# Kernel optimization log

Hardware: AMD Instinct MI355X
Metric: run time of the kernel (lower is better)

Reference implementation:

```python
import jax, jax.numpy as jnp
import numpy as np

TEMPERATURE = 100.0  # exponential-smoothing temperature from __init__ default
ETA = 1.0            # feature/label cost tradeoff


def _cdist(a, b):
    # Euclidean distance matrix [M, N] between rows of a [M, D] and b [N, D]
    sq = (jnp.sum(a * a, axis=1)[:, None]
          + jnp.sum(b * b, axis=1)[None, :]
          - 2.0 * (a @ b.T))
    return jnp.sqrt(jnp.maximum(sq, 1e-12))


def setup_inputs() -> dict:
    key = jax.random.key(0)
    ks = jax.random.split(key, 9)
    B, Nt, Ns, H, Wd, C = 1024, 8192, 8192, 32, 32, 10
    D = H * Wd
    x = jax.random.normal(ks[0], (B, H, Wd), jnp.float32)
    target_features = jax.random.normal(ks[1], (Nt, H, Wd), jnp.float32)
    aligned_source_features = jax.random.normal(ks[2], (Nt, H, Wd), jnp.float32)
    source_features = jax.random.normal(ks[3], (Ns, H, Wd), jnp.float32)
    source_high_dim_labels = jax.random.uniform(ks[4], (Ns, C), jnp.float32)
    aligned_target_labels = jax.random.uniform(ks[5], (Ns, C), jnp.float32)
    source_label_distances = jax.random.uniform(ks[6], (C, C), jnp.float32)
    W = jax.random.normal(ks[7], (D, C), jnp.float32) * 0.02
    b = jnp.zeros((C,), jnp.float32)
    return {
        "x": x,
        "target_features": target_features,
        "aligned_source_features": aligned_source_features,
        "source_features": source_features,
        "source_high_dim_labels": source_high_dim_labels,
        "aligned_target_labels": aligned_target_labels,
        "source_label_distances": source_label_distances,
        "W": W,
        "b": b,
    }


def reference(x, target_features, aligned_source_features, source_features,
              source_high_dim_labels, aligned_target_labels,
              source_label_distances, W, b):
    B = x.shape[0]
    xf = x.reshape(B, -1)                                   # [B, D]
    tf = target_features.reshape(target_features.shape[0], -1)       # [Nt, D]
    asf = aligned_source_features.reshape(aligned_source_features.shape[0], -1)  # [Nt, D]
    sf = source_features.reshape(source_features.shape[0], -1)       # [Ns, D]

    # --- feature transport: target -> source (plain_softmax) ---
    d_feat = _cdist(xf, tf)                                 # [B, Nt]
    w_feat = jax.nn.softmax(-TEMPERATURE * d_feat, axis=1)  # [B, Nt]
    x_src = w_feat @ asf                                    # [B, D] in source space

    # --- source model (linear classifier head -> soft predictions) ---
    preds = jax.nn.softmax(x_src @ W + b, axis=1)           # [B, C]

    # --- label transport: source -> target (plain_softmax) ---
    cost = _cdist(x_src, sf)                                # feature_dists=True: [B, Ns]
    # label_dists=True: cost of moving predicted label mass to each sample's label
    cost = cost + ETA * (preds @ source_label_distances @ source_high_dim_labels.T)
    w_lab = jax.nn.softmax(-TEMPERATURE * cost, axis=1)     # [B, Ns]
    y = w_lab @ aligned_target_labels                       # [B, C] in target label space
    return y
```

## Files before the change

### kernel.cpp

```cpp
#include <hip/hip_runtime.h>
#include <hip/hip_bf16.h>
#include <math.h>

#define B_ROWS 1024
#define NT 8192
#define NS 8192
#define DIM 1024
#define NC 10
#define TEMP 100.0f
#define WCAP 1024

typedef __bf16 bf16x8 __attribute__((ext_vector_type(8)));
typedef __bf16 bf16x4 __attribute__((ext_vector_type(4)));
typedef float f32x4 __attribute__((ext_vector_type(4)));

#define GLOAD_LDS(g, l) \
    __builtin_amdgcn_global_load_lds((__attribute__((address_space(1))) void*)(g), \
                                     (__attribute__((address_space(3))) void*)(l), 16, 0, 0)

__device__ inline __bf16 split_hi(float v) { return (__bf16)v; }
__device__ inline __bf16 split_lo(float v) {
    __bf16 h = (__bf16)v;
    return (__bf16)(v - (float)h);
}

__device__ inline float wave_max(float v) {
    #pragma unroll
    for (int off = 32; off > 0; off >>= 1)
        v = fmaxf(v, __shfl_down(v, off, 64));
    return v;
}
__device__ inline float wave_sum(float v) {
    #pragma unroll
    for (int off = 32; off > 0; off >>= 1)
        v += __shfl_down(v, off, 64);
    return v;
}

__device__ inline void conv_norm_row(const float* __restrict__ X, int row,
                                     __bf16* __restrict__ X2,
                                     float* __restrict__ norms,
                                     float* sred) {
    int c = threadIdx.x * 4;
    float4 v = *(const float4*)(X + (size_t)row * DIM + c);
    bf16x4 h, l;
    h[0] = split_hi(v.x); l[0] = split_lo(v.x);
    h[1] = split_hi(v.y); l[1] = split_lo(v.y);
    h[2] = split_hi(v.z); l[2] = split_lo(v.z);
    h[3] = split_hi(v.w); l[3] = split_lo(v.w);
    *(bf16x4*)(X2 + (size_t)row * 2048 + c) = h;
    *(bf16x4*)(X2 + (size_t)row * 2048 + 1024 + c) = l;
    float acc = v.x * v.x + v.y * v.y + v.z * v.z + v.w * v.w;
    float w = wave_sum(acc);
    int lane = threadIdx.x & 63, wid = threadIdx.x >> 6;
    if (lane == 0) sred[wid] = w;
    __syncthreads();
    if (threadIdx.x == 0) norms[row] = sred[0] + sred[1] + sred[2] + sred[3];
}

__global__ __launch_bounds__(256) void k_prep0(const float* __restrict__ x,
                                               const float* __restrict__ tf,
                                               const float* __restrict__ sf,
                                               const float* __restrict__ sld,
                                               const float* __restrict__ shdl,
                                               const float* __restrict__ atl,
                                               __bf16* __restrict__ x2,
                                               __bf16* __restrict__ tf2,
                                               __bf16* __restrict__ sf2,
                                               float* __restrict__ nx_,
                                               float* __restrict__ nt_,
                                               float* __restrict__ ns_,
                                               float* __restrict__ M2Tt,
                                               float* __restrict__ atlt) {
    __shared__ float sred[4];
    __shared__ float sldL[NC * NC];
    int b = blockIdx.x;
    if (b < B_ROWS) {
        conv_norm_row(x, b, x2, nx_, sred);
    } else if (b < B_ROWS + NT) {
        conv_norm_row(tf, b - B_ROWS, tf2, nt_, sred);
    } else if (b < B_ROWS + NT + NS) {
        conv_norm_row(sf, b - B_ROWS - NT, sf2, ns_, sred);
    } else {
        if (threadIdx.x < NC * NC) sldL[threadIdx.x] = sld[threadIdx.x];
        __syncthreads();
        int j = (b - B_ROWS - NT - NS) * 256 + threadIdx.x;
        float sh[NC], at[NC];
        #pragma unroll
        for (int k = 0; k < NC; k++) sh[k] = shdl[(size_t)j * NC + k];
        #pragma unroll
        for (int c = 0; c < NC; c++) at[c] = atl[(size_t)j * NC + c];
        #pragma unroll
        for (int c = 0; c < NC; c++) {
            float t = 0.f;
            #pragma unroll
            for (int k = 0; k < NC; k++) t += sldL[c * NC + k] * sh[k];
            M2Tt[c * NS + j] = t;
            atlt[c * NS + j] = at[c];
        }
    }
}

template <bool LOGITS>
__global__ __launch_bounds__(256) void k_gemm3(const __bf16* __restrict__ A2,
                                               const __bf16* __restrict__ B2,
                                               float* __restrict__ C,
                                               int M, int N, int K, int ksplit,
                                               const float* __restrict__ rowN,
                                               const float* __restrict__ colN) {
    __shared__ unsigned short AhS[8192], AlS[8192], BhS[8192], BlS[8192];
    __shared__ float extraL[LOGITS ? 256 : 2];
    float* rnL = extraL;
    float* cnL = extraL + 128;

    int tid = threadIdx.x;
    int wid = tid >> 6, lane = tid & 63;
    int wm = (wid >> 1) * 64, wn = (wid & 1) * 64;
    int id = blockIdx.y * gridDim.x + blockIdx.x;
    int bn_i = ((id >> 6) << 3) | (id & 7);
    int bm_i = (id >> 3) & 7;
    int bm = bm_i * 128, bn = bn_i * 128;
    size_t K2 = 2 * (size_t)K;
    int k_begin = blockIdx.z * ksplit;
    int nsteps = ksplit >> 6;

    if (LOGITS) {
        if (tid < 128) rnL[tid] = rowN[bm + tid];
        else cnL[tid - 128] = colN[bn + tid - 128];
    }

    f32x4 acc[4][4];
    #pragma unroll
    for (int i = 0; i < 4; i++)
        #pragma unroll
        for (int j = 0; j < 4; j++) acc[i][j] = (f32x4){0.f, 0.f, 0.f, 0.f};

    int r_in = lane >> 3;
    int cgo = ((lane & 7) ^ r_in) * 8;
    const __bf16* gA = A2 + (size_t)(bm + wid * 32 + r_in) * K2 + k_begin + cgo;
    const __bf16* gB = B2 + (size_t)(bn + wid * 32 + r_in) * K2 + k_begin + cgo;
    char* AhB = (char*)AhS; char* AlB = (char*)AlS;
    char* BhB = (char*)BhS; char* BlB = (char*)BlS;
    int lbw = wid * 4096;
    size_t row8 = 8 * K2;

    int ra = lane & 15, q = lane >> 4;
    int aoff[4][2], boff[4][2];
    #pragma unroll
    for (int i = 0; i < 4; i++) {
        #pragma unroll
        for (int kh = 0; kh < 2; kh++) {
            int chunk = ((kh << 2) | q) ^ (ra & 7);
            aoff[i][kh] = (wm + i * 16 + ra) * 64 + chunk * 8;
            boff[i][kh] = (wn + i * 16 + ra) * 64 + chunk * 8;
        }
    }
    const __bf16* AhE = (const __bf16*)AhS;
    const __bf16* AlE = (const __bf16*)AlS;
    const __bf16* BhE = (const __bf16*)BhS;
    const __bf16* BlE = (const __bf16*)BlS;

    for (int ks = 0; ks < nsteps; ks++) {
        __syncthreads();
        #pragma unroll
        for (int p = 0; p < 4; p++) {
            size_t go = p * row8;
            int lo = lbw + p * 1024;
            GLOAD_LDS(gA + go, AhB + lo);
            GLOAD_LDS(gA + go + K, AlB + lo);
            GLOAD_LDS(gB + go, BhB + lo);
            GLOAD_LDS(gB + go + K, BlB + lo);
        }
        gA += 64; gB += 64;
        __syncthreads();

        #pragma unroll
        for (int kh = 0; kh < 2; kh++) {
            bf16x8 ah[4], al[4];
            #pragma unroll
            for (int mi = 0; mi < 4; mi++) {
                ah[mi] = *(const bf16x8*)(AhE + aoff[mi][kh]);
                al[mi] = *(const bf16x8*)(AlE + aoff[mi][kh]);
            }
            #pragma unroll
            for (int ni = 0; ni < 4; ni++) {
                bf16x8 bh = *(const bf16x8*)(BhE + boff[ni][kh]);
                bf16x8 bl = *(const bf16x8*)(BlE + boff[ni][kh]);
                #pragma unroll
                for (int mi = 0; mi < 4; mi++) {
                    acc[mi][ni] = __builtin_amdgcn_mfma_f32_16x16x32_bf16(ah[mi], bh, acc[mi][ni], 0, 0, 0);
                    acc[mi][ni] = __builtin_amdgcn_mfma_f32_16x16x32_bf16(ah[mi], bl, acc[mi][ni], 0, 0, 0);
                    acc[mi][ni] = __builtin_amdgcn_mfma_f32_16x16x32_bf16(al[mi], bh, acc[mi][ni], 0, 0, 0);
                }
            }
        }
    }

    if (!LOGITS) {
        float* Cb = C + (size_t)blockIdx.z * M * N;
        #pragma unroll
        for (int mi = 0; mi < 4; mi++) {
            #pragma unroll
            for (int ni = 0; ni < 4; ni++) {
                int r0 = bm + wm + mi * 16 + q * 4;
                int c0 = bn + wn + ni * 16 + ra;
                Cb[(size_t)(r0 + 0) * N + c0] = acc[mi][ni][0];
                Cb[(size_t)(r0 + 1) * N + c0] = acc[mi][ni][1];
                Cb[(size_t)(r0 + 2) * N + c0] = acc[mi][ni][2];
                Cb[(size_t)(r0 + 3) * N + c0] = acc[mi][ni][3];
            }
        }
    } else {
        #pragma unroll
        for (int mi = 0; mi < 4; mi++) {
            #pragma unroll
            for (int ni = 0; ni < 4; ni++) {
                int cl = wn + ni * 16 + ra;
                float cn = cnL[cl];
                #pragma unroll
                for (int i = 0; i < 4; i++) {
                    int rl = wm + mi * 16 + q * 4 + i;
                    float sq = rnL[rl] + cn - 2.f * acc[mi][ni][i];
                    float d = sqrtf(fmaxf(sq, 1e-12f));
                    C[(size_t)(bm + rl) * N + bn + cl] = -TEMP * d;
                }
            }
        }
    }
}

__global__ __launch_bounds__(256) void k_xsrc(const float* __restrict__ S,
                                              const float* __restrict__ asf,
                                              const float* __restrict__ W,
                                              const float* __restrict__ bias,
                                              __bf16* __restrict__ xsrc2,
                                              float* __restrict__ nx2_,
                                              float* __restrict__ preds) {
    __shared__ float sm[4];
    __shared__ float ss[4];
    __shared__ int   sidx[WCAP];
    __shared__ float swt[WCAP];
    __shared__ int   scnt;
    __shared__ float red[4][NC + 1];
    int row = blockIdx.x;
    int tid = threadIdx.x;
    int lane = tid & 63, wid = tid >> 6;
    if (tid == 0) scnt = 0;
    const float4* sr = (const float4*)(S + (size_t)row * NT);
    float4 vals[NT / 1024];
    float lmax = -1e30f;
    #pragma unroll
    for (int u = 0; u < NT / 1024; u++) {
        float4 v = sr[tid + u * 256];
        vals[u] = v;
        lmax = fmaxf(fmaxf(fmaxf(v.x, v.y), fmaxf(v.z, v.w)), lmax);
    }
    float wmx = wave_max(lmax);
    if (lane == 0) sm[wid] = wmx;
    __syncthreads();
    float bmax = fmaxf(fmaxf(sm[0], sm[1]), fmaxf(sm[2], sm[3]));
    float lsum = 0.f;
    #pragma unroll
    for (int u = 0; u < NT / 1024; u++) {
        float4 v = vals[u];
        v.x = __expf(v.x - bmax); v.y = __expf(v.y - bmax);
        v.z = __expf(v.z - bmax); v.w = __expf(v.w - bmax);
        vals[u] = v;
        lsum += v.x + v.y + v.z + v.w;
    }
    float wsv = wave_sum(lsum);
    if (lane == 0) ss[wid] = wsv;
    __syncthreads();
    float bsum = ss[0] + ss[1] + ss[2] + ss[3];
    float inv = 1.0f / bsum;
    float thr = 1e-8f * bsum;
    #pragma unroll
    for (int u = 0; u < NT / 1024; u++) {
        float4 v = vals[u];
        int j = (tid + u * 256) * 4;
        if (v.x > thr) { int k = atomicAdd(&scnt, 1); if (k < WCAP) { sidx[k] = j;     swt[k] = v.x * inv; } }
        if (v.y > thr) { int k = atomicAdd(&scnt, 1); if (k < WCAP) { sidx[k] = j + 1; swt[k] = v.y * inv; } }
        if (v.z > thr) { int k = atomicAdd(&scnt, 1); if (k < WCAP) { sidx[k] = j + 2; swt[k] = v.z * inv; } }
        if (v.w > thr) { int k = atomicAdd(&scnt, 1); if (k < WCAP) { sidx[k] = j + 3; swt[k] = v.w * inv; } }
    }
    __syncthreads();
    int cnt = scnt < WCAP ? scnt : WCAP;
    int c = tid * 4;
    float sx = 0.f, sy = 0.f, sz = 0.f, sw = 0.f;
    for (int i = 0; i < cnt; i++) {
        float wg = swt[i];
        float4 v = *(const float4*)(asf + (size_t)sidx[i] * DIM + c);
        sx += wg * v.x; sy += wg * v.y; sz += wg * v.z; sw += wg * v.w;
    }
    bf16x4 h, l;
    h[0] = split_hi(sx); l[0] = split_lo(sx);
    h[1] = split_hi(sy); l[1] = split_lo(sy);
    h[2] = split_hi(sz); l[2] = split_lo(sz);
    h[3] = split_hi(sw); l[3] = split_lo(sw);
    *(bf16x4*)(xsrc2 + (size_t)row * 2048 + c) = h;
    *(bf16x4*)(xsrc2 + (size_t)row * 2048 + 1024 + c) = l;
    float accn = sx * sx + sy * sy + sz * sz + sw * sw;
    float accp[NC];
    #pragma unroll
    for (int cc = 0; cc < NC; cc++)
        accp[cc] = sx * W[(c + 0) * NC + cc] + sy * W[(c + 1) * NC + cc]
                 + sz * W[(c + 2) * NC + cc] + sw * W[(c + 3) * NC + cc];
    accn = wave_sum(accn);
    #pragma unroll
    for (int cc = 0; cc < NC; cc++) accp[cc] = wave_sum(accp[cc]);
    if (lane == 0) {
        red[wid][0] = accn;
        #pragma unroll
        for (int cc = 0; cc < NC; cc++) red[wid][1 + cc] = accp[cc];
    }
    __syncthreads();
    if (tid == 0) {
        nx2_[row] = red[0][0] + red[1][0] + red[2][0] + red[3][0];
        float lo[NC];
        float m = -1e30f;
        #pragma unroll
        for (int cc = 0; cc < NC; cc++) {
            lo[cc] = red[0][1 + cc] + red[1][1 + cc] + red[2][1 + cc] + red[3][1 + cc]
                   + bias[cc];
            m = fmaxf(m, lo[cc]);
        }
        float ssum = 0.f;
        #pragma unroll
        for (int cc = 0; cc < NC; cc++) {
            lo[cc] = __expf(lo[cc] - m);
            ssum += lo[cc];
        }
        float iv = 1.0f / ssum;
        #pragma unroll
        for (int cc = 0; cc < NC; cc++) preds[(size_t)row * NC + cc] = lo[cc] * iv;
    }
}

__global__ __launch_bounds__(256) void k_lab_softmax_y(const float* __restrict__ S,
                                                       const float* __restrict__ predsG,
                                                       const float* __restrict__ M2Tt,
                                                       const float* __restrict__ atlt,
                                                       float* __restrict__ y) {
    int r0 = blockIdx.x * 2, r1 = r0 + 1;
    float pr0[NC], pr1[NC];
    #pragma unroll
    for (int c = 0; c < NC; c++) {
        pr0[c] = predsG[(size_t)r0 * NC + c];
        pr1[c] = predsG[(size_t)r1 * NC + c];
    }
    const float4* s0 = (const float4*)(S + (size_t)r0 * NS);
    const float4* s1 = (const float4*)(S + (size_t)r1 * NS);
    const float4* M2 = (const float4*)M2Tt;
    const float4* AT = (const float4*)atlt;
    float4 v0[NS / 1024], v1[NS / 1024];
    float m0 = -1e30f, m1 = -1e30f;
    #pragma unroll
    for (int u = 0; u < NS / 1024; u++) {
        int j4 = threadIdx.x + u * 256;
        float4 a = s0[j4], b = s1[j4];
        float4 lab0 = make_float4(0.f, 0.f, 0.f, 0.f);
        float4 lab1 = make_float4(0.f, 0.f, 0.f, 0.f);
        #pragma unroll
        for (int c = 0; c < NC; c++) {
            float4 mv = M2[c * 2048 + j4];
            lab0.x += pr0[c] * mv.x; lab0.y += pr0[c] * mv.y;
            lab0.z += pr0[c] * mv.z; lab0.w += pr0[c] * mv.w;
            lab1.x += pr1[c] * mv.x; lab1.y += pr1[c] * mv.y;
            lab1.z += pr1[c] * mv.z; lab1.w += pr1[c] * mv.w;
        }
        a.x -= TEMP * lab0.x; a.y -= TEMP * lab0.y;
        a.z -= TEMP * lab0.z; a.w -= TEMP * lab0.w;
        b.x -= TEMP * lab1.x; b.y -= TEMP * lab1.y;
        b.z -= TEMP * lab1.z; b.w -= TEMP * lab1.w;
        v0[u] = a; v1[u] = b;
        m0 = fmaxf(m0, fmaxf(fmaxf(a.x, a.y), fmaxf(a.z, a.w)));
        m1 = fmaxf(m1, fmaxf(fmaxf(b.x, b.y), fmaxf(b.z, b.w)));
    }
    __shared__ float sm[2][4];
    __shared__ float ss[2][4];
    __shared__ float yred[4][2][NC];
    int lane = threadIdx.x & 63, wid = threadIdx.x >> 6;
    float wm0 = wave_max(m0), wm1 = wave_max(m1);
    if (lane == 0) { sm[0][wid] = wm0; sm[1][wid] = wm1; }
    __syncthreads();
    float bm0 = fmaxf(fmaxf(sm[0][0], sm[0][1]), fmaxf(sm[0][2], sm[0][3]));
    float bm1 = fmaxf(fmaxf(sm[1][0], sm[1][1]), fmaxf(sm[1][2], sm[1][3]));
    float ls0 = 0.f, ls1 = 0.f;
    #pragma unroll
    for (int u = 0; u < NS / 1024; u++) {
        float4 a = v0[u], b = v1[u];
        a.x = __expf(a.x - bm0); a.y = __expf(a.y - bm0);
        a.z = __expf(a.z - bm0); a.w = __expf(a.w - bm0);
        b.x = __expf(b.x - bm1); b.y = __expf(b.y - bm1);
        b.z = __expf(b.z - bm1); b.w = __expf(b.w - bm1);
        v0[u] = a; v1[u] = b;
        ls0 += a.x + a.y + a.z + a.w;
        ls1 += b.x + b.y + b.z + b.w;
    }
    float ws0 = wave_sum(ls0), ws1 = wave_sum(ls1);
    if (lane == 0) { ss[0][wid] = ws0; ss[1][wid] = ws1; }
    __syncthreads();
    float inv0 = 1.0f / (ss[0][0] + ss[0][1] + ss[0][2] + ss[0][3]);
    float inv1 = 1.0f / (ss[1][0] + ss[1][1] + ss[1][2] + ss[1][3]);
    float y0[NC] = {}, y1[NC] = {};
    #pragma unroll
    for (int u = 0; u < NS / 1024; u++) {
        int j4 = threadIdx.x + u * 256;
        float4 a = v0[u], b = v1[u];
        #pragma unroll
        for (int c = 0; c < NC; c++) {
            float4 av = AT[c * 2048 + j4];
            y0[c] += a.x * av.x + a.y * av.y + a.z * av.z + a.w * av.w;
            y1[c] += b.x * av.x + b.y * av.y + b.z * av.z + b.w * av.w;
        }
    }
    #pragma unroll
    for (int c = 0; c < NC; c++) {
        y0[c] = wave_sum(y0[c]) * inv0;
        y1[c] = wave_sum(y1[c]) * inv1;
    }
    if (lane == 0) {
        #pragma unroll
        for (int c = 0; c < NC; c++) { yred[wid][0][c] = y0[c]; yred[wid][1][c] = y1[c]; }
    }
    __syncthreads();
    if (threadIdx.x < 2 * NC) {
        int r = threadIdx.x / NC, c = threadIdx.x - r * NC;
        y[(size_t)(r0 + r) * NC + c] = yred[0][r][c] + yred[1][r][c] + yred[2][r][c] + yred[3][r][c];
    }
}

extern "C" void kernel_launch(void* const* d_in, const int* in_sizes, int n_in,
                              void* d_out, int out_size, void* d_ws, size_t ws_size,
                              hipStream_t stream) {
    const float* x    = (const float*)d_in[0];
    const float* tf   = (const float*)d_in[1];
    const float* asf  = (const float*)d_in[2];
    const float* sf   = (const float*)d_in[3];
    const float* shdl = (const float*)d_in[4];
    const float* atl  = (const float*)d_in[5];
    const float* sld  = (const float*)d_in[6];
    const float* W    = (const float*)d_in[7];
    const float* bias = (const float*)d_in[8];
    float* y = (float*)d_out;

    char* wsb = (char*)d_ws;
    float*  S     = (float*)(wsb);
    __bf16* tf2   = (__bf16*)(wsb + (32u << 20));
    __bf16* sf2   = (__bf16*)(wsb + (64u << 20));
    __bf16* x2    = (__bf16*)(wsb + (96u << 20));
    __bf16* xsrc2 = (__bf16*)(wsb + (100u << 20));
    float*  nt_   = (float*)(wsb + (108u << 20));
    float*  ns_   = nt_ + NT;
    float*  nx_   = ns_ + NS;
    float*  nx2_  = nx_ + B_ROWS;
    float*  preds = nx2_ + B_ROWS;
    float*  M2Tt  = preds + B_ROWS * NC;
    float*  atlt  = M2Tt + NS * NC;

    k_prep0<<<B_ROWS + NT + NS + NS / 256, 256, 0, stream>>>(x, tf, sf, sld, shdl, atl,
                                                             x2, tf2, sf2, nx_, nt_, ns_,
                                                             M2Tt, atlt);

    {
        dim3 g(NT / 128, B_ROWS / 128, 1);
        k_gemm3<true><<<g, 256, 0, stream>>>(x2, tf2, S, B_ROWS, NT, DIM, DIM,
                                             nx_, nt_);
    }

    k_xsrc<<<B_ROWS, 256, 0, stream>>>(S, asf, W, bias, xsrc2, nx2_, preds);

    {
        dim3 g(NS / 128, B_ROWS / 128, 1);
        k_gemm3<true><<<g, 256, 0, stream>>>(xsrc2, sf2, S, B_ROWS, NS, DIM, DIM,
                                             nx2_, ns_);
    }
    k_lab_softmax_y<<<B_ROWS / 2, 256, 0, stream>>>(S, preds, M2Tt, atlt, y);
}
```

Measured before the change: 265.6 us.

## Halve GEMM K-step to shrink LDS and raise occupancy with k-major layout

The split-bf16 GEMM kernel now stages 32-wide K slices instead of 64, halving shared memory per block and adding a min-blocks-per-SM launch bound of 4. The LDS tile moves to a k-chunk-major layout where each wave loads one of the four hi/lo arrays row-per-lane, which drops the XOR swizzle and precomputed offsets. The goal is higher occupancy to hide load latency. In exchange it needs twice as many barrier-separated steps, less MFMA work per sync, and the unswizzled layout may cause LDS bank conflicts or uncoalesced global loads, since each lane reads a different row.

```diff
diff --git a/kernel.cpp b/kernel.cpp
--- a/kernel.cpp
+++ b/kernel.cpp
@@ -102,13 +102,13 @@
 }
 
 template <bool LOGITS>
-__global__ __launch_bounds__(256) void k_gemm3(const __bf16* __restrict__ A2,
-                                               const __bf16* __restrict__ B2,
-                                               float* __restrict__ C,
-                                               int M, int N, int K, int ksplit,
-                                               const float* __restrict__ rowN,
-                                               const float* __restrict__ colN) {
-    __shared__ unsigned short AhS[8192], AlS[8192], BhS[8192], BlS[8192];
+__global__ __launch_bounds__(256, 4) void k_gemm3(const __bf16* __restrict__ A2,
+                                                  const __bf16* __restrict__ B2,
+                                                  float* __restrict__ C,
+                                                  int M, int N, int K, int ksplit,
+                                                  const float* __restrict__ rowN,
+                                                  const float* __restrict__ colN) {
+    __shared__ unsigned short AhS[4096], AlS[4096], BhS[4096], BlS[4096];
     __shared__ float extraL[LOGITS ? 256 : 2];
     float* rnL = extraL;
     float* cnL = extraL + 128;
@@ -122,7 +122,7 @@
     int bm = bm_i * 128, bn = bn_i * 128;
     size_t K2 = 2 * (size_t)K;
     int k_begin = blockIdx.z * ksplit;
-    int nsteps = ksplit >> 6;
+    int nsteps = ksplit >> 5;
 
     if (LOGITS) {
         if (tid < 128) rnL[tid] = rowN[bm + tid];
@@ -135,63 +135,47 @@
         #pragma unroll
         for (int j = 0; j < 4; j++) acc[i][j] = (f32x4){0.f, 0.f, 0.f, 0.f};
 
-    int r_in = lane >> 3;
-    int cgo = ((lane & 7) ^ r_in) * 8;
-    const __bf16* gA = A2 + (size_t)(bm + wid * 32 + r_in) * K2 + k_begin + cgo;
-    const __bf16* gB = B2 + (size_t)(bn + wid * 32 + r_in) * K2 + k_begin + cgo;
-    char* AhB = (char*)AhS; char* AlB = (char*)AlS;
-    char* BhB = (char*)BhS; char* BlB = (char*)BlS;
-    int lbw = wid * 4096;
-    size_t row8 = 8 * K2;
+    char* arrB = (wid == 0) ? (char*)AhS : (wid == 1) ? (char*)AlS
+               : (wid == 2) ? (char*)BhS : (char*)BlS;
+    const __bf16* gbase = (wid < 2) ? A2 : B2;
+    int rbase = (wid < 2) ? bm : bn;
+    const __bf16* g0 = gbase + (size_t)(rbase + lane) * K2 + ((wid & 1) ? K : 0) + k_begin;
+    size_t off64 = (size_t)64 * K2;
 
     int ra = lane & 15, q = lane >> 4;
-    int aoff[4][2], boff[4][2];
-    #pragma unroll
-    for (int i = 0; i < 4; i++) {
-        #pragma unroll
-        for (int kh = 0; kh < 2; kh++) {
-            int chunk = ((kh << 2) | q) ^ (ra & 7);
-            aoff[i][kh] = (wm + i * 16 + ra) * 64 + chunk * 8;
-            boff[i][kh] = (wn + i * 16 + ra) * 64 + chunk * 8;
-        }
-    }
     const __bf16* AhE = (const __bf16*)AhS;
     const __bf16* AlE = (const __bf16*)AlS;
     const __bf16* BhE = (const __bf16*)BhS;
     const __bf16* BlE = (const __bf16*)BlS;
+    int qo = q * 1024;
 
     for (int ks = 0; ks < nsteps; ks++) {
         __syncthreads();
         #pragma unroll
-        for (int p = 0; p < 4; p++) {
-            size_t go = p * row8;
-            int lo = lbw + p * 1024;
-            GLOAD_LDS(gA + go, AhB + lo);
-            GLOAD_LDS(gA + go + K, AlB + lo);
-            GLOAD_LDS(gB + go, BhB + lo);
-            GLOAD_LDS(gB + go + K, BlB + lo);
-        }
-        gA += 64; gB += 64;
+        for (int p = 0; p < 8; p++) {
+            int c = p >> 1, h = p & 1;
+            GLOAD_LDS(g0 + (size_t)h * off64 + c * 8, arrB + c * 2048 + h * 1024);
+        }
+        g0 += 32;
         __syncthreads();
 
-        #pragma unroll
-        for (int kh = 0; kh < 2; kh++) {
-            bf16x8 ah[4], al[4];
+        bf16x8 ah[4], al[4];
+        #pragma unroll
+        for (int mi = 0; mi < 4; mi++) {
+            int ro = qo + (wm + mi * 16 + ra) * 8;
+            ah[mi] = *(const bf16x8*)(AhE + ro);
+            al[mi] = *(const bf16x8*)(AlE + ro);
+        }
+        #pragma unroll
+        for (int ni = 0; ni < 4; ni++) {
+            int ro = qo + (wn + ni * 16 + ra) * 8;
+            bf16x8 bh = *(const bf16x8*)(BhE + ro);
+            bf16x8 bl = *(const bf16x8*)(BlE + ro);
             #pragma unroll
             for (int mi = 0; mi < 4; mi++) {
-                ah[mi] = *(const bf16x8*)(AhE + aoff[mi][kh]);
-                al[mi] = *(const bf16x8*)(AlE + aoff[mi][kh]);
-            }
-            #pragma unroll
-            for (int ni = 0; ni < 4; ni++) {
-                bf16x8 bh = *(const bf16x8*)(BhE + boff[ni][kh]);
-                bf16x8 bl = *(const bf16x8*)(BlE + boff[ni][kh]);
-                #pragma unroll
-                for (int mi = 0; mi < 4; mi++) {
-                    acc[mi][ni] = __builtin_amdgcn_mfma_f32_16x16x32_bf16(ah[mi], bh, acc[mi][ni], 0, 0, 0);
-                    acc[mi][ni] = __builtin_amdgcn_mfma_f32_16x16x32_bf16(ah[mi], bl, acc[mi][ni], 0, 0, 0);
-                    acc[mi][ni] = __builtin_amdgcn_mfma_f32_16x16x32_bf16(al[mi], bh, acc[mi][ni], 0, 0, 0);
-                }
+                acc[mi][ni] = __builtin_amdgcn_mfma_f32_16x16x32_bf16(ah[mi], bh, acc[mi][ni], 0, 0, 0);
+                acc[mi][ni] = __builtin_amdgcn_mfma_f32_16x16x32_bf16(ah[mi], bl, acc[mi][ni], 0, 0, 0);
+                acc[mi][ni] = __builtin_amdgcn_mfma_f32_16x16x32_bf16(al[mi], bh, acc[mi][ni], 0, 0, 0);
             }
         }
     }
```

Measured after the change: 463.9 us. 74.6% more time.

## Double-buffer LDS tiles in split-bf16 GEMM to overlap loads with MFMA

Applied to the files above, without the earlier changes.

The GEMM kernel now keeps two LDS buffers per operand (hi/lo for A and B). While MFMAs consume the current buffer, it issues direct global-to-LDS loads for the next k-step into the other buffer. This replaces the two barriers per step with a single barrier at the end of each step, so memory latency can be hidden behind compute. The cost is doubled LDS use (about 128KB per block), which likely cuts the blocks resident per CU and hence occupancy.

```diff
diff --git a/kernel.cpp b/kernel.cpp
--- a/kernel.cpp
+++ b/kernel.cpp
@@ -108,7 +108,7 @@
                                                int M, int N, int K, int ksplit,
                                                const float* __restrict__ rowN,
                                                const float* __restrict__ colN) {
-    __shared__ unsigned short AhS[8192], AlS[8192], BhS[8192], BlS[8192];
+    __shared__ unsigned short AhS[2][8192], AlS[2][8192], BhS[2][8192], BlS[2][8192];
     __shared__ float extraL[LOGITS ? 256 : 2];
     float* rnL = extraL;
     float* cnL = extraL + 128;
@@ -139,8 +139,6 @@
     int cgo = ((lane & 7) ^ r_in) * 8;
     const __bf16* gA = A2 + (size_t)(bm + wid * 32 + r_in) * K2 + k_begin + cgo;
     const __bf16* gB = B2 + (size_t)(bn + wid * 32 + r_in) * K2 + k_begin + cgo;
-    char* AhB = (char*)AhS; char* AlB = (char*)AlS;
-    char* BhB = (char*)BhS; char* BlB = (char*)BlS;
     int lbw = wid * 4096;
     size_t row8 = 8 * K2;
 
@@ -155,24 +153,34 @@
             boff[i][kh] = (wn + i * 16 + ra) * 64 + chunk * 8;
         }
     }
-    const __bf16* AhE = (const __bf16*)AhS;
-    const __bf16* AlE = (const __bf16*)AlS;
-    const __bf16* BhE = (const __bf16*)BhS;
-    const __bf16* BlE = (const __bf16*)BlS;
-
+
+#define STAGE3(buf, koff) do {                                                 \
+        const __bf16* _a = gA + (size_t)(koff);                                \
+        const __bf16* _b = gB + (size_t)(koff);                                \
+        char* _Ah = (char*)&AhS[buf][0]; char* _Al = (char*)&AlS[buf][0];      \
+        char* _Bh = (char*)&BhS[buf][0]; char* _Bl = (char*)&BlS[buf][0];      \
+        _Pragma("unroll")                                                      \
+        for (int p = 0; p < 4; p++) {                                          \
+            size_t go = p * row8;                                              \
+            int lo = lbw + p * 1024;                                           \
+            GLOAD_LDS(_a + go, _Ah + lo);                                      \
+            GLOAD_LDS(_a + go + K, _Al + lo);                                  \
+            GLOAD_LDS(_b + go, _Bh + lo);                                      \
+            GLOAD_LDS(_b + go + K, _Bl + lo);                                  \
+        }                                                                      \
+    } while (0)
+
+    STAGE3(0, 0);
+    __syncthreads();
+
+    int cur = 0;
     for (int ks = 0; ks < nsteps; ks++) {
-        __syncthreads();
-        #pragma unroll
-        for (int p = 0; p < 4; p++) {
-            size_t go = p * row8;
-            int lo = lbw + p * 1024;
-            GLOAD_LDS(gA + go, AhB + lo);
-            GLOAD_LDS(gA + go + K, AlB + lo);
-            GLOAD_LDS(gB + go, BhB + lo);
-            GLOAD_LDS(gB + go + K, BlB + lo);
-        }
-        gA += 64; gB += 64;
-        __syncthreads();
+        if (ks + 1 < nsteps) STAGE3(cur ^ 1, (size_t)(ks + 1) * 64);
+
+        const __bf16* AhE = (const __bf16*)&AhS[cur][0];
+        const __bf16* AlE = (const __bf16*)&AlS[cur][0];
+        const __bf16* BhE = (const __bf16*)&BhS[cur][0];
+        const __bf16* BlE = (const __bf16*)&BlS[cur][0];
 
         #pragma unroll
         for (int kh = 0; kh < 2; kh++) {
@@ -194,7 +202,10 @@
                 }
             }
         }
-    }
+        __syncthreads();
+        cur ^= 1;
+    }
+#undef STAGE3
 
     if (!LOGITS) {
         float* Cb = C + (size_t)blockIdx.z * M * N;
```

New measurement: 309.2 us. +16.4%, slower.
